# Optimization experiments

Hardware: AMD Instinct MI355X
Metric: run time of the kernel (lower is better)

The kernel has to match this reference:

```python
import math
import jax, jax.numpy as jnp
import numpy as np

D, H, NB, L, K = 45, 256, 6, 2, 8          # features, hidden, maf blocks, made hidden layers, spline bins
M = 3 * K - 1                               # params per feature (tails='linear')
TAIL = -math.log(1e-6)                      # tail_bound = -log(alpha)
MIN_BW = MIN_BH = MIN_D = 1e-3


def _masks():
    # nflows MADE sequential degrees (random_mask=False)
    d_in = np.arange(1, D + 1)
    d_h = (np.arange(H) % (D - 1)) + 1
    m0 = (d_h[:, None] >= d_in[None, :]).astype(np.float32)   # [H, D]
    mh = (d_h[:, None] >= d_h[None, :]).astype(np.float32)    # [H, H]
    d_out = np.repeat(d_in, M)                                 # nflows tile(): each degree repeated M times
    mf = (d_out[:, None] > d_h[None, :]).astype(np.float32)   # [D*M, H], strict for output layer
    return jnp.asarray(m0), jnp.asarray(mh), jnp.asarray(mf)


def _rq_spline(x, params):
    # x: [B, D]; params: [B, D, M]. unconstrained_rational_quadratic_spline, tails='linear'.
    uw = params[..., :K] / math.sqrt(H)        # nflows divides by sqrt(hidden_features)
    uh = params[..., K:2 * K] / math.sqrt(H)
    const = math.log(math.exp(1.0 - MIN_D) - 1.0)
    ud = jnp.pad(params[..., 2 * K:], ((0, 0), (0, 0), (1, 1)), constant_values=const)  # [B,D,K+1]
    inside = (x >= -TAIL) & (x <= TAIL)
    xc = jnp.clip(x, -TAIL, TAIL)

    def bin_edges(u, mn):
        p = jax.nn.softmax(u, -1)
        p = mn + (1.0 - mn * K) * p
        c = jnp.pad(jnp.cumsum(p, -1), ((0, 0), (0, 0), (1, 0)))
        c = 2.0 * TAIL * c - TAIL
        c = c.at[..., 0].set(-TAIL).at[..., -1].set(TAIL)
        return c, c[..., 1:] - c[..., :-1]

    cw, w = bin_edges(uw, MIN_BW)              # cumwidths [B,D,K+1], widths [B,D,K]
    ch, h = bin_edges(uh, MIN_BH)
    d = MIN_D + jax.nn.softplus(ud)            # derivatives [B,D,K+1]

    idx = jnp.clip(jnp.sum((xc[..., None] >= cw), -1) - 1, 0, K - 1)[..., None]
    g = lambda a: jnp.take_along_axis(a, idx, -1)[..., 0]
    icw, ibw, ich, ih = g(cw[..., :-1]), g(w), g(ch[..., :-1]), g(h)
    idelta = g(h / w)
    id0, id1 = g(d[..., :-1]), g(d[..., 1:])

    th = (xc - icw) / ibw
    th1 = th * (1.0 - th)
    den = idelta + (id0 + id1 - 2.0 * idelta) * th1
    y = ich + ih * (idelta * th * th + id0 * th1) / den
    lad = jnp.log(idelta * idelta * (id1 * th * th + 2.0 * idelta * th1 + id0 * (1.0 - th) ** 2)) - 2.0 * jnp.log(den)
    return jnp.where(inside, y, x), jnp.where(inside, lad, 0.0)


def setup_inputs() -> dict:
    key = jax.random.key(0)
    ks = jax.random.split(key, 10)
    B, s = 32768, 0.02
    return {
        "x": jax.random.normal(ks[0], (B, D), jnp.float32),
        "cond": jax.random.normal(ks[1], (B, 1), jnp.float32),
        "W0": jax.random.normal(ks[2], (NB, H, D), jnp.float32) * s,
        "b0": jax.random.normal(ks[3], (NB, H), jnp.float32) * s,
        "Wc": jax.random.normal(ks[4], (NB, H, 1), jnp.float32) * s,
        "bc": jax.random.normal(ks[5], (NB, H), jnp.float32) * s,
        "Wh": jax.random.normal(ks[6], (NB, L, H, H), jnp.float32) * s,
        "bh": jax.random.normal(ks[7], (NB, L, H), jnp.float32) * s,
        "Wf": jax.random.normal(ks[8], (NB, D * M, H), jnp.float32) * s,
        "bf": jax.random.normal(ks[9], (NB, D * M), jnp.float32) * s,
    }


def reference(x, cond, W0, b0, Wc, bc, Wh, bh, Wf, bf):
    m0, mh, mf = _masks()
    z = x
    ld = jnp.zeros(x.shape[0], x.dtype)
    for b in range(NB):  # CompositeTransform of NB MAF blocks
        hid = z @ (W0[b] * m0).T + b0[b] + cond @ Wc[b].T + bc[b]
        for l in range(L):  # MaskedFeedforwardBlock: linear -> ReLU (dropout=0, no BN)
            hid = jax.nn.relu(hid @ (Wh[b, l] * mh).T + bh[b, l])
        params = (hid @ (Wf[b] * mf).T + bf[b]).reshape(z.shape[0], D, M)
        z, lad = _rq_spline(z, params)
        ld = ld + lad.sum(-1)
    log_z = 0.5 * D * math.log(2.0 * math.pi)
    return -0.5 * jnp.sum(z * z, axis=1) - log_z + ld
```

## Files before the change

kernel.cpp:

```cpp
#include <hip/hip_runtime.h>


typedef __bf16 bf16;
typedef __bf16 bf16x8 __attribute__((ext_vector_type(8)));
typedef float  f32x16 __attribute__((ext_vector_type(16)));

#define TAILF  13.815510557964274f
#define LOGZ   41.352233994210265f

#define WS_W0M   0
#define WS_WHM   196608
#define WS_WFM   1769472
#define WS_BEFF  5210112
#define WS_BFP   5216256
#define WS_WCC   5243136
#define WS_NEED  5249280

#define N_W0  (6*256*64)
#define N_WH  (6*2*256*256)
#define N_WF  (6*5*224*256)
#define N_PREP (N_W0 + N_WH + N_WF)

__global__ void prep_all(const float* __restrict__ W0, const float* __restrict__ b0,
                         const float* __restrict__ Wc, const float* __restrict__ bc,
                         const float* __restrict__ Wh, const float* __restrict__ Wf,
                         const float* __restrict__ bfv,
                         bf16* __restrict__ W0m, bf16* __restrict__ Whm,
                         bf16* __restrict__ Wfm,
                         float* __restrict__ beff, float* __restrict__ bfp,
                         float* __restrict__ Wcc)
{
    int idx = blockIdx.x * 256 + threadIdx.x;
    if (idx < N_W0) {
        int j = idx & 7, lane = (idx >> 3) & 63, chunk = idx >> 9;
        int kt = chunk & 3, cg = (chunk >> 2) & 7, b = chunk >> 5;
        int col = cg * 32 + (lane & 31);
        int k   = kt * 16 + (lane >> 5) * 8 + j;
        float v = 0.f;
        if (k < 45 && (col % 44) >= k)
            v = W0[(b * 256 + col) * 45 + k];
        W0m[idx] = (bf16)v;
        if (k == 0) {
            beff[b * 256 + col] = b0[b * 256 + col] + bc[b * 256 + col];
            Wcc[b * 256 + col]  = Wc[b * 256 + col];
        }
    } else if (idx < N_W0 + N_WH) {
        int id = idx - N_W0;
        int j = id & 7, lane = (id >> 3) & 63, chunk = id >> 9;
        int kt = chunk & 15, cg = (chunk >> 4) & 7, bl = chunk >> 7;
        int col = cg * 32 + (lane & 31);
        int k   = kt * 16 + (lane >> 5) * 8 + j;
        float v = ((col % 44) >= (k % 44)) ? Wh[bl * 65536 + col * 256 + k] : 0.f;
        Whm[id] = (bf16)v;
    } else if (idx < N_PREP) {
        int id = idx - (N_W0 + N_WH);
        int j = id & 7, lane = (id >> 3) & 63, chunk = id >> 9;
        int kt = chunk & 15, t2 = chunk >> 4;
        int cg = t2 % 7, bg = t2 / 7;
        int b  = bg / 5, g = bg - 5 * b;
        int col = cg * 32 + (lane & 31);
        int k   = kt * 16 + (lane >> 5) * 8 + j;
        int f   = 9 * g + col / 23;
        int m   = col - (col / 23) * 23;
        bool valid = (col < 207);
        float v = 0.f;
        if (valid && (f > (k % 44)))
            v = Wf[(b * 1035 + f * 23 + m) * 256 + k];
        Wfm[id] = (bf16)v;
        if (k == 0)
            bfp[bg * 224 + col] = valid ? bfv[b * 1035 + f * 23 + m] : 0.f;
    }
}

#define SO_ZF    0
#define SO_ZB    11776
#define SO_HIDA  20992
#define SO_PBUF  54784
#define SO_COND  81408
#define SO_LD    81664
#define SMEM_BYTES 81920

template<int KT, int NACT, int MODE, int LIMIT>
__device__ __forceinline__ void gemm32(
    const bf16* Asrc, int lda,
    const bf16* __restrict__ Wp,
    const float* __restrict__ bias, const float* __restrict__ wcol,
    const float* condl, bf16* dst, int ldd,
    int w, int lane, bool preEpiSync)
{
    const bool act  = (w < NACT);
    const int  l31  = lane & 31;
    const int  kh8  = (lane >> 5) * 8;
    const bf16* Bp  = Wp + ((size_t)w * KT) * 512 + lane * 8;
    const bf16* Ap  = Asrc + l31 * lda + kh8;

    f32x16 acc0 = {}, acc1 = {};
    constexpr int CH = (KT < 8) ? KT : 8;
    #pragma unroll
    for (int khb = 0; khb < KT / CH; ++khb) {
        bf16x8 bq[CH];
        if (act) {
            #pragma unroll
            for (int c = 0; c < CH; ++c)
                bq[c] = *reinterpret_cast<const bf16x8*>(Bp + (khb * CH + c) * 512);
            #pragma unroll
            for (int c = 0; c < CH; ++c) {
                int kt = khb * CH + c;
                bf16x8 a0 = *reinterpret_cast<const bf16x8*>(Ap + kt * 16);
                bf16x8 a1 = *reinterpret_cast<const bf16x8*>(Ap + 32 * lda + kt * 16);
                acc0 = __builtin_amdgcn_mfma_f32_32x32x16_bf16(a0, bq[c], acc0, 0, 0, 0);
                acc1 = __builtin_amdgcn_mfma_f32_32x32x16_bf16(a1, bq[c], acc1, 0, 0, 0);
            }
        }
    }

    if (preEpiSync) __syncthreads();

    if (act) {
        const int col = w * 32 + l31;
        if (NACT == 8 || col < LIMIT) {
            const float bv  = bias[col];
            const float wcv = (MODE == 0) ? wcol[col] : 0.f;
            #pragma unroll
            for (int r = 0; r < 16; ++r) {
                int row = (r & 3) + 8 * (r >> 2) + (kh8 >> 1);
                float v0 = acc0[r] + bv;
                float v1 = acc1[r] + bv;
                if (MODE == 0) { v0 += condl[row] * wcv; v1 += condl[row + 32] * wcv; }
                if (MODE == 1) { v0 = fmaxf(v0, 0.f);   v1 = fmaxf(v1, 0.f); }
                dst[row * ldd + col]        = (bf16)v0;
                dst[(row + 32) * ldd + col] = (bf16)v1;
            }
        }
    }
    __syncthreads();
}

template<int NF>
__device__ __forceinline__ void do_spline(int fb, float* zf, bf16* zb,
                                          const bf16* pbuf, float* ldl, int t)
{
    for (int task = t; task < 64 * NF; task += 512) {
        int r  = task / NF;
        int fl = task - r * NF;
        const bf16* pp = pbuf + r * 208 + fl * 23;
        float P[23];
        #pragma unroll
        for (int m = 0; m < 23; ++m) P[m] = (float)pp[m];

        float xin = zf[r * 46 + fb + fl];
        float xc  = fminf(fmaxf(xin, -TAILF), TAILF);
        bool inside = (xin >= -TAILF) && (xin <= TAILF);

        float mw = P[0];
        #pragma unroll
        for (int i = 1; i < 8; ++i) mw = fmaxf(mw, P[i]);
        float ew[8], sw = 0.f;
        #pragma unroll
        for (int i = 0; i < 8; ++i) { ew[i] = __expf((P[i] - mw) * 0.0625f); sw += ew[i]; }
        float rws = 0.992f / sw;
        float cw[9]; cw[0] = -TAILF;
        #pragma unroll
        for (int i = 0; i < 8; ++i)
            cw[i + 1] = cw[i] + 2.f * TAILF * (1e-3f + ew[i] * rws);
        cw[8] = TAILF;
        float wb[8];
        #pragma unroll
        for (int i = 0; i < 8; ++i) wb[i] = cw[i + 1] - cw[i];

        float mh = P[8];
        #pragma unroll
        for (int i = 1; i < 8; ++i) mh = fmaxf(mh, P[8 + i]);
        float eh[8], sh = 0.f;
        #pragma unroll
        for (int i = 0; i < 8; ++i) { eh[i] = __expf((P[8 + i] - mh) * 0.0625f); sh += eh[i]; }
        float rhs = 0.992f / sh;
        float ch[9]; ch[0] = -TAILF;
        #pragma unroll
        for (int i = 0; i < 8; ++i)
            ch[i + 1] = ch[i] + 2.f * TAILF * (1e-3f + eh[i] * rhs);
        ch[8] = TAILF;
        float hb[8];
        #pragma unroll
        for (int i = 0; i < 8; ++i) hb[i] = ch[i + 1] - ch[i];

        float dd[9];
        dd[0] = 1.0f; dd[8] = 1.0f;
        #pragma unroll
        for (int i = 1; i < 8; ++i)
            dd[i] = 1e-3f + __logf(1.f + __expf(P[15 + i]));

        float icw = cw[0], ich = ch[0], ibw = wb[0], ibh = hb[0];
        float id0 = dd[0], id1 = dd[1];
        #pragma unroll
        for (int i = 1; i < 8; ++i) {
            bool ge = xc >= cw[i];
            icw = ge ? cw[i] : icw;  ich = ge ? ch[i] : ich;
            ibw = ge ? wb[i] : ibw;  ibh = ge ? hb[i] : ibh;
            id0 = ge ? dd[i] : id0;  id1 = ge ? dd[i + 1] : id1;
        }

        float th  = (xc - icw) / ibw;
        float th1 = th * (1.f - th);
        float dl  = ibh / ibw;
        float den = dl + (id0 + id1 - 2.f * dl) * th1;
        float yy  = ich + ibh * (dl * th * th + id0 * th1) / den;
        float num = dl * dl * (id1 * th * th + 2.f * dl * th1
                               + id0 * (1.f - th) * (1.f - th));
        float lad = __logf(num) - 2.f * __logf(den);

        if (inside) {
            zf[r * 46 + fb + fl] = yy;
            zb[r * 72 + fb + fl] = (bf16)yy;
            atomicAdd(&ldl[r], lad);
        }
    }
}

__global__ __launch_bounds__(512, 4) void maf_main(
    const float* __restrict__ x, const float* __restrict__ cond,
    const float* __restrict__ bh_all,
    const bf16* __restrict__ W0m, const bf16* __restrict__ Whm,
    const bf16* __restrict__ Wfm,
    const float* __restrict__ beff, const float* __restrict__ bfp,
    const float* __restrict__ Wcc,
    float* __restrict__ out, int B)
{
    extern __shared__ char smem[];
    float* zf    = (float*)(smem + SO_ZF);
    bf16*  zb    = (bf16*)(smem + SO_ZB);
    bf16*  hidA  = (bf16*)(smem + SO_HIDA);
    bf16*  pbuf  = (bf16*)(smem + SO_PBUF);
    float* condl = (float*)(smem + SO_COND);
    float* ldl   = (float*)(smem + SO_LD);

    const int t    = threadIdx.x;
    const int r0   = blockIdx.x * 64;
    const int w    = t >> 6;
    const int lane = t & 63;

    for (int i = t; i < 64 * 27; i += 512) {
        int r = i / 27, c = i - (i / 27) * 27;
        zb[r * 72 + 45 + c] = (bf16)0.f;
    }
    for (int i = t; i < 64 * 45; i += 512) {
        int r = i / 45, f = i - (i / 45) * 45;
        float v = (r0 + r < B) ? x[(size_t)(r0 + r) * 45 + f] : 0.f;
        zf[r * 46 + f] = v;
        zb[r * 72 + f] = (bf16)v;
    }
    if (t < 64) {
        condl[t] = (r0 + t < B) ? cond[r0 + t] : 0.f;
        ldl[t]   = 0.f;
    }
    __syncthreads();

    #pragma unroll 1
    for (int b = 0; b < 6; ++b) {
        gemm32<4, 8, 0, 256>(zb, 72, W0m + b * 16384,
                             beff + b * 256, Wcc + b * 256, condl,
                             hidA, 264, w, lane, false);
        #pragma unroll 1
        for (int l = 0; l < 2; ++l)
            gemm32<16, 8, 1, 256>(hidA, 264, Whm + (b * 2 + l) * 65536,
                                  bh_all + (b * 2 + l) * 256, nullptr, condl,
                                  hidA, 264, w, lane, true);
        #pragma unroll 1
        for (int g = 0; g < 5; ++g) {
            gemm32<16, 7, 2, 208>(hidA, 264, Wfm + (size_t)(b * 5 + g) * 57344,
                                  bfp + (b * 5 + g) * 224, nullptr, condl,
                                  pbuf, 208, w, lane, false);
            do_spline<9>(g * 9, zf, zb, pbuf, ldl, t);
            __syncthreads();
        }
    }

    if (t < 64 && r0 + t < B) {
        float s = 0.f;
        #pragma unroll
        for (int f = 0; f < 45; ++f) { float v = zf[t * 46 + f]; s += v * v; }
        out[r0 + t] = -0.5f * s - LOGZ + ldl[t];
    }
}

extern "C" void kernel_launch(void* const* d_in, const int* in_sizes, int n_in,
                              void* d_out, int out_size, void* d_ws, size_t ws_size,
                              hipStream_t stream)
{
    const float* x    = (const float*)d_in[0];
    const float* cond = (const float*)d_in[1];
    const float* W0   = (const float*)d_in[2];
    const float* b0   = (const float*)d_in[3];
    const float* Wc   = (const float*)d_in[4];
    const float* bc   = (const float*)d_in[5];
    const float* Wh   = (const float*)d_in[6];
    const float* bh   = (const float*)d_in[7];
    const float* Wf   = (const float*)d_in[8];
    const float* bfv  = (const float*)d_in[9];
    float* out = (float*)d_out;

    const int B = in_sizes[0] / 45;
    if (ws_size < (size_t)WS_NEED) return;

    char* ws = (char*)d_ws;
    bf16*  W0m  = (bf16*)(ws + WS_W0M);
    bf16*  Whm  = (bf16*)(ws + WS_WHM);
    bf16*  Wfm  = (bf16*)(ws + WS_WFM);
    float* beff = (float*)(ws + WS_BEFF);
    float* bfp  = (float*)(ws + WS_BFP);
    float* Wcc  = (float*)(ws + WS_WCC);

    prep_all<<<(N_PREP + 255) / 256, 256, 0, stream>>>(
        W0, b0, Wc, bc, Wh, Wf, bfv, W0m, Whm, Wfm, beff, bfp, Wcc);

    (void)hipFuncSetAttribute((const void*)maf_main,
                              hipFuncAttributeMaxDynamicSharedMemorySize,
                              SMEM_BYTES);

    const int nwg = (B + 63) / 64;
    maf_main<<<nwg, 512, SMEM_BYTES, stream>>>(
        x, cond, bh, W0m, Whm, Wfm, beff, bfp, Wcc, out, B);
}
```

Before: 372.9 us.

## Permute MADE hidden units by degree and skip masked-zero K tiles with balanced wave schedule

Hidden units are reordered so their MADE degrees are sorted, which turns the masked weight matrices into block-triangular form. Each GEMM now skips the k-tiles that are entirely zero, and per-wave schedule tables in constant memory spread the remaining tiles evenly across the 8 waves. The spline parameter buffer is also re-laid out so each thread reads 16-byte vectors, and per-row log-det sums go to a register instead of a shared atomic on every feature. The cost is more complex prep indexing, hand-tuned schedule tables that must match the masks exactly, and a runtime trip count in the inner loop.

```diff
diff --git a/kernel.cpp b/kernel.cpp
--- a/kernel.cpp
+++ b/kernel.cpp
@@ -14,21 +14,32 @@
 #define WS_BEFF  5210112
 #define WS_BFP   5216256
 #define WS_WCC   5243136
-#define WS_NEED  5249280
+#define WS_BHP   5249280
+#define WS_NEED  5261568
 
 #define N_W0  (6*256*64)
 #define N_WH  (6*2*256*256)
 #define N_WF  (6*5*224*256)
 #define N_PREP (N_W0 + N_WH + N_WF)
 
+__device__ __forceinline__ int s_deg(int s) {
+    return (s < 216) ? (s / 6) : (36 + (s - 216) / 5);
+}
+__device__ __forceinline__ int s_orig(int s) {
+    int d, rk;
+    if (s < 216) { d = s / 6; rk = s - d * 6; }
+    else { int u = s - 216; d = 36 + u / 5; rk = u - (u / 5) * 5; }
+    return d + 44 * rk;
+}
+
 __global__ void prep_all(const float* __restrict__ W0, const float* __restrict__ b0,
                          const float* __restrict__ Wc, const float* __restrict__ bc,
                          const float* __restrict__ Wh, const float* __restrict__ Wf,
-                         const float* __restrict__ bfv,
+                         const float* __restrict__ bfv, const float* __restrict__ bh,
                          bf16* __restrict__ W0m, bf16* __restrict__ Whm,
                          bf16* __restrict__ Wfm,
                          float* __restrict__ beff, float* __restrict__ bfp,
-                         float* __restrict__ Wcc)
+                         float* __restrict__ Wcc, float* __restrict__ bhp)
 {
     int idx = blockIdx.x * 256 + threadIdx.x;
     if (idx < N_W0) {
@@ -36,13 +47,14 @@
         int kt = chunk & 3, cg = (chunk >> 2) & 7, b = chunk >> 5;
         int col = cg * 32 + (lane & 31);
         int k   = kt * 16 + (lane >> 5) * 8 + j;
+        int o   = s_orig(col);
         float v = 0.f;
-        if (k < 45 && (col % 44) >= k)
-            v = W0[(b * 256 + col) * 45 + k];
+        if (k < 45 && s_deg(col) >= k)
+            v = W0[(b * 256 + o) * 45 + k];
         W0m[idx] = (bf16)v;
         if (k == 0) {
-            beff[b * 256 + col] = b0[b * 256 + col] + bc[b * 256 + col];
-            Wcc[b * 256 + col]  = Wc[b * 256 + col];
+            beff[b * 256 + col] = b0[b * 256 + o] + bc[b * 256 + o];
+            Wcc[b * 256 + col]  = Wc[b * 256 + o];
         }
     } else if (idx < N_W0 + N_WH) {
         int id = idx - N_W0;
@@ -50,8 +62,11 @@
         int kt = chunk & 15, cg = (chunk >> 4) & 7, bl = chunk >> 7;
         int col = cg * 32 + (lane & 31);
         int k   = kt * 16 + (lane >> 5) * 8 + j;
-        float v = ((col % 44) >= (k % 44)) ? Wh[bl * 65536 + col * 256 + k] : 0.f;
+        int oc  = s_orig(col), ok = s_orig(k);
+        float v = (s_deg(col) >= s_deg(k)) ? Wh[bl * 65536 + oc * 256 + ok] : 0.f;
         Whm[id] = (bf16)v;
+        if (k == 0)
+            bhp[bl * 256 + col] = bh[bl * 256 + oc];
     } else if (idx < N_PREP) {
         int id = idx - (N_W0 + N_WH);
         int j = id & 7, lane = (id >> 3) & 63, chunk = id >> 9;
@@ -60,12 +75,13 @@
         int b  = bg / 5, g = bg - 5 * b;
         int col = cg * 32 + (lane & 31);
         int k   = kt * 16 + (lane >> 5) * 8 + j;
+        int ok  = s_orig(k);
         int f   = 9 * g + col / 23;
         int m   = col - (col / 23) * 23;
         bool valid = (col < 207);
         float v = 0.f;
-        if (valid && (f > (k % 44)))
-            v = Wf[(b * 1035 + f * 23 + m) * 256 + k];
+        if (valid && (f > s_deg(k)))
+            v = Wf[(b * 1035 + f * 23 + m) * 256 + ok];
         Wfm[id] = (bf16)v;
         if (k == 0)
             bfp[bg * 224 + col] = valid ? bfv[b * 1035 + f * 23 + m] : 0.f;
@@ -74,79 +90,141 @@
 
 #define SO_ZF    0
 #define SO_ZB    11776
-#define SO_HIDA  20992
-#define SO_PBUF  54784
-#define SO_COND  81408
-#define SO_LD    81664
-#define SMEM_BYTES 81920
-
-template<int KT, int NACT, int MODE, int LIMIT>
+#define SO_HIDA  18944
+#define SO_PBUF  52736
+#define SO_COND  80528
+#define SO_LD    80784
+#define SMEM_BYTES 81040
+
+#define PBF 1544
+
+#define E2(c0,h0,k0,c1,h1,k1) \
+    ( (unsigned)(((k0)<<8)|((h0)<<5)|(c0)) | ((unsigned)(((k1)<<8)|((h1)<<5)|(c1))<<16) )
+
+__constant__ unsigned SCHED_IN[8] = {
+    E2(6,0,3, 0,0,1), E2(6,1,3, 0,1,1), E2(7,0,3, 1,0,1), E2(7,1,3, 1,1,1),
+    E2(3,0,2, 2,0,1), E2(3,1,2, 2,1,1), E2(4,0,2, 5,0,2), E2(4,1,2, 5,1,2)
+};
+__constant__ unsigned SCHED_HID[8] = {
+    E2(7,0,16, 0,0,3), E2(7,1,16, 0,1,3), E2(6,0,15, 1,0,5), E2(6,1,15, 1,1,5),
+    E2(5,0,12, 2,0,6), E2(5,1,12, 2,1,6), E2(4,0,11, 3,0,9), E2(4,1,11, 3,1,9)
+};
+__constant__ unsigned SCHED_OUT[5][8] = {
+  { E2(4,0,3, 0,0,1),  E2(4,1,3, 0,1,1),  E2(5,0,3, 1,0,1),  E2(5,1,3, 1,1,1),
+    E2(6,0,3, 31,0,0), E2(6,1,3, 31,0,0), E2(2,0,2, 2,1,2),  E2(3,0,2, 3,1,2) },
+  { E2(5,0,7, 0,0,4),  E2(5,1,7, 0,1,4),  E2(6,0,7, 31,0,0), E2(6,1,7, 31,0,0),
+    E2(3,0,6, 1,0,5),  E2(3,1,6, 1,1,5),  E2(4,0,6, 2,0,5),  E2(4,1,6, 2,1,5) },
+  { E2(5,0,10, 0,0,8), E2(5,1,10, 0,1,8), E2(6,0,10, 1,0,8), E2(6,1,10, 1,1,8),
+    E2(2,0,9, 2,1,9),  E2(3,0,9, 3,1,9),  E2(4,0,9, 31,0,0), E2(4,1,9, 31,0,0) },
+  { E2(5,0,14, 0,0,11),E2(5,1,14, 0,1,11),E2(6,0,14, 31,0,0),E2(6,1,14, 31,0,0),
+    E2(4,0,13, 1,0,11),E2(4,1,13, 1,1,11),E2(2,0,12, 2,1,12),E2(3,0,12, 3,1,12) },
+  { E2(3,0,16, 0,0,14),E2(3,1,16, 0,1,14),E2(4,0,16, 1,0,15),E2(4,1,16, 1,1,15),
+    E2(5,0,16, 2,0,15),E2(5,1,16, 2,1,15),E2(6,0,16, 31,0,0),E2(6,1,16, 31,0,0) }
+};
+
+template<int MODE>
+__device__ __forceinline__ void epi32(const f32x16& acc, int cg, int hf,
+    const float* __restrict__ bias, const float* __restrict__ wcol,
+    const float* condl, bf16* dst, int l31, int kh8)
+{
+    const int col = cg * 32 + l31;
+    if (MODE == 2 && col >= 207) return;
+    const float bv = bias[col];
+    const int rb = (kh8 >> 1) + hf * 32;
+    if (MODE == 2) {
+        const int fl = col / 23, m = col - fl * 23;
+        bf16* dp = dst + fl * PBF + m;
+        #pragma unroll
+        for (int r = 0; r < 16; ++r) {
+            int row = (r & 3) + 8 * (r >> 2) + rb;
+            dp[row * 24] = (bf16)(acc[r] + bv);
+        }
+    } else {
+        const float wcv = (MODE == 0) ? wcol[col] : 0.f;
+        #pragma unroll
+        for (int r = 0; r < 16; ++r) {
+            int row = (r & 3) + 8 * (r >> 2) + rb;
+            float v = acc[r] + bv;
+            if (MODE == 0) v += condl[row] * wcv;
+            if (MODE == 1) v = fmaxf(v, 0.f);
+            dst[row * 264 + col] = (bf16)v;
+        }
+    }
+}
+
+template<int KTFULL, int MODE>
 __device__ __forceinline__ void gemm32(
-    const bf16* Asrc, int lda,
+    const bf16* Asrc, const int lda,
     const bf16* __restrict__ Wp,
     const float* __restrict__ bias, const float* __restrict__ wcol,
-    const float* condl, bf16* dst, int ldd,
+    const float* condl, bf16* dst,
+    const unsigned* __restrict__ sched,
     int w, int lane, bool preEpiSync)
 {
-    const bool act  = (w < NACT);
-    const int  l31  = lane & 31;
-    const int  kh8  = (lane >> 5) * 8;
-    const bf16* Bp  = Wp + ((size_t)w * KT) * 512 + lane * 8;
-    const bf16* Ap  = Asrc + l31 * lda + kh8;
+    const int l31 = lane & 31;
+    const int kh8 = (lane >> 5) * 8;
+    const unsigned se = sched[__builtin_amdgcn_readfirstlane(w)];
+    const int cg0 = se & 31,         hf0 = (se >> 5) & 1,  kt0 = (se >> 8) & 31;
+    const int cg1 = (se >> 16) & 31, hf1 = (se >> 21) & 1, kt1 = (se >> 24) & 31;
 
     f32x16 acc0 = {}, acc1 = {};
-    constexpr int CH = (KT < 8) ? KT : 8;
-    #pragma unroll
-    for (int khb = 0; khb < KT / CH; ++khb) {
-        bf16x8 bq[CH];
-        if (act) {
+    {
+        const bf16* Bp = Wp + (size_t)cg0 * (KTFULL * 512) + lane * 8;
+        const bf16* Ap = Asrc + (hf0 * 32 + l31) * lda + kh8;
+        #pragma unroll 1
+        for (int kb = 0; kb < kt0; kb += 4) {
+            bf16x8 bq[4], aq[4];
             #pragma unroll
-            for (int c = 0; c < CH; ++c)
-                bq[c] = *reinterpret_cast<const bf16x8*>(Bp + (khb * CH + c) * 512);
+            for (int c = 0; c < 4; ++c) if (kb + c < kt0) {
+                bq[c] = *reinterpret_cast<const bf16x8*>(Bp + (kb + c) * 512);
+                aq[c] = *reinterpret_cast<const bf16x8*>(Ap + (kb + c) * 16);
+            }
             #pragma unroll
-            for (int c = 0; c < CH; ++c) {
-                int kt = khb * CH + c;
-                bf16x8 a0 = *reinterpret_cast<const bf16x8*>(Ap + kt * 16);
-                bf16x8 a1 = *reinterpret_cast<const bf16x8*>(Ap + 32 * lda + kt * 16);
-                acc0 = __builtin_amdgcn_mfma_f32_32x32x16_bf16(a0, bq[c], acc0, 0, 0, 0);
-                acc1 = __builtin_amdgcn_mfma_f32_32x32x16_bf16(a1, bq[c], acc1, 0, 0, 0);
+            for (int c = 0; c < 4; ++c) if (kb + c < kt0)
+                acc0 = __builtin_amdgcn_mfma_f32_32x32x16_bf16(aq[c], bq[c], acc0, 0, 0, 0);
+        }
+    }
+    {
+        const bf16* Bp = Wp + (size_t)cg1 * (KTFULL * 512) + lane * 8;
+        const bf16* Ap = Asrc + (hf1 * 32 + l31) * lda + kh8;
+        #pragma unroll 1
+        for (int kb = 0; kb < kt1; kb += 4) {
+            bf16x8 bq[4], aq[4];
+            #pragma unroll
+            for (int c = 0; c < 4; ++c) if (kb + c < kt1) {
+                bq[c] = *reinterpret_cast<const bf16x8*>(Bp + (kb + c) * 512);
+                aq[c] = *reinterpret_cast<const bf16x8*>(Ap + (kb + c) * 16);
             }
+            #pragma unroll
+            for (int c = 0; c < 4; ++c) if (kb + c < kt1)
+                acc1 = __builtin_amdgcn_mfma_f32_32x32x16_bf16(aq[c], bq[c], acc1, 0, 0, 0);
         }
     }
 
     if (preEpiSync) __syncthreads();
 
-    if (act) {
-        const int col = w * 32 + l31;
-        if (NACT == 8 || col < LIMIT) {
-            const float bv  = bias[col];
-            const float wcv = (MODE == 0) ? wcol[col] : 0.f;
-            #pragma unroll
-            for (int r = 0; r < 16; ++r) {
-                int row = (r & 3) + 8 * (r >> 2) + (kh8 >> 1);
-                float v0 = acc0[r] + bv;
-                float v1 = acc1[r] + bv;
-                if (MODE == 0) { v0 += condl[row] * wcv; v1 += condl[row + 32] * wcv; }
-                if (MODE == 1) { v0 = fmaxf(v0, 0.f);   v1 = fmaxf(v1, 0.f); }
-                dst[row * ldd + col]        = (bf16)v0;
-                dst[(row + 32) * ldd + col] = (bf16)v1;
-            }
-        }
-    }
+    if (cg0 != 31) epi32<MODE>(acc0, cg0, hf0, bias, wcol, condl, dst, l31, kh8);
+    if (cg1 != 31) epi32<MODE>(acc1, cg1, hf1, bias, wcol, condl, dst, l31, kh8);
     __syncthreads();
 }
 
-template<int NF>
-__device__ __forceinline__ void do_spline(int fb, float* zf, bf16* zb,
-                                          const bf16* pbuf, float* ldl, int t)
-{
-    for (int task = t; task < 64 * NF; task += 512) {
-        int r  = task / NF;
-        int fl = task - r * NF;
-        const bf16* pp = pbuf + r * 208 + fl * 23;
+__device__ __forceinline__ void do_spline9(int fb, float* zf, bf16* zb,
+                                           const bf16* pbuf, int t, float& lad_acc)
+{
+    #pragma unroll 1
+    for (int task = t; task < 576; task += 512) {
+        int fl = task >> 6, r = task & 63;
+        const bf16* pp = pbuf + fl * PBF + r * 24;
+        bf16x8 q0 = *reinterpret_cast<const bf16x8*>(pp);
+        bf16x8 q1 = *reinterpret_cast<const bf16x8*>(pp + 8);
+        bf16x8 q2 = *reinterpret_cast<const bf16x8*>(pp + 16);
         float P[23];
         #pragma unroll
-        for (int m = 0; m < 23; ++m) P[m] = (float)pp[m];
+        for (int m = 0; m < 8; ++m) P[m]      = (float)q0[m];
+        #pragma unroll
+        for (int m = 0; m < 8; ++m) P[8 + m]  = (float)q1[m];
+        #pragma unroll
+        for (int m = 0; m < 7; ++m) P[16 + m] = (float)q2[m];
 
         float xin = zf[r * 46 + fb + fl];
         float xc  = fminf(fmaxf(xin, -TAILF), TAILF);
@@ -211,19 +289,18 @@
 
         if (inside) {
             zf[r * 46 + fb + fl] = yy;
-            zb[r * 72 + fb + fl] = (bf16)yy;
-            atomicAdd(&ldl[r], lad);
-        }
+            zb[r * 56 + fb + fl] = (bf16)yy;
+        }
+        lad_acc += inside ? lad : 0.f;
     }
 }
 
 __global__ __launch_bounds__(512, 4) void maf_main(
     const float* __restrict__ x, const float* __restrict__ cond,
-    const float* __restrict__ bh_all,
     const bf16* __restrict__ W0m, const bf16* __restrict__ Whm,
     const bf16* __restrict__ Wfm,
     const float* __restrict__ beff, const float* __restrict__ bfp,
-    const float* __restrict__ Wcc,
+    const float* __restrict__ Wcc, const float* __restrict__ bhp,
     float* __restrict__ out, int B)
 {
     extern __shared__ char smem[];
@@ -239,15 +316,15 @@
     const int w    = t >> 6;
     const int lane = t & 63;
 
-    for (int i = t; i < 64 * 27; i += 512) {
-        int r = i / 27, c = i - (i / 27) * 27;
-        zb[r * 72 + 45 + c] = (bf16)0.f;
+    for (int i = t; i < 64 * 11; i += 512) {
+        int r = i / 11, c = i - (i / 11) * 11;
+        zb[r * 56 + 45 + c] = (bf16)0.f;
     }
     for (int i = t; i < 64 * 45; i += 512) {
         int r = i / 45, f = i - (i / 45) * 45;
         float v = (r0 + r < B) ? x[(size_t)(r0 + r) * 45 + f] : 0.f;
         zf[r * 46 + f] = v;
-        zb[r * 72 + f] = (bf16)v;
+        zb[r * 56 + f] = (bf16)v;
     }
     if (t < 64) {
         condl[t] = (r0 + t < B) ? cond[r0 + t] : 0.f;
@@ -255,25 +332,30 @@
     }
     __syncthreads();
 
+    float lad_acc = 0.f;
+
     #pragma unroll 1
     for (int b = 0; b < 6; ++b) {
-        gemm32<4, 8, 0, 256>(zb, 72, W0m + b * 16384,
-                             beff + b * 256, Wcc + b * 256, condl,
-                             hidA, 264, w, lane, false);
+        gemm32<4, 0>(zb, 56, W0m + b * 16384,
+                     beff + b * 256, Wcc + b * 256, condl,
+                     hidA, SCHED_IN, w, lane, false);
         #pragma unroll 1
         for (int l = 0; l < 2; ++l)
-            gemm32<16, 8, 1, 256>(hidA, 264, Whm + (b * 2 + l) * 65536,
-                                  bh_all + (b * 2 + l) * 256, nullptr, condl,
-                                  hidA, 264, w, lane, true);
+            gemm32<16, 1>(hidA, 264, Whm + (b * 2 + l) * 65536,
+                          bhp + (b * 2 + l) * 256, nullptr, condl,
+                          hidA, SCHED_HID, w, lane, true);
         #pragma unroll 1
         for (int g = 0; g < 5; ++g) {
-            gemm32<16, 7, 2, 208>(hidA, 264, Wfm + (size_t)(b * 5 + g) * 57344,
-                                  bfp + (b * 5 + g) * 224, nullptr, condl,
-                                  pbuf, 208, w, lane, false);
-            do_spline<9>(g * 9, zf, zb, pbuf, ldl, t);
+            gemm32<16, 2>(hidA, 264, Wfm + (size_t)(b * 5 + g) * 57344,
+                          bfp + (b * 5 + g) * 224, nullptr, condl,
+                          pbuf, SCHED_OUT[g], w, lane, false);
+            do_spline9(g * 9, zf, zb, pbuf, t, lad_acc);
             __syncthreads();
         }
     }
+
+    atomicAdd(&ldl[t & 63], lad_acc);
+    __syncthreads();
 
     if (t < 64 && r0 + t < B) {
         float s = 0.f;
@@ -309,9 +391,10 @@
     float* beff = (float*)(ws + WS_BEFF);
     float* bfp  = (float*)(ws + WS_BFP);
     float* Wcc  = (float*)(ws + WS_WCC);
+    float* bhp  = (float*)(ws + WS_BHP);
 
     prep_all<<<(N_PREP + 255) / 256, 256, 0, stream>>>(
-        W0, b0, Wc, bc, Wh, Wf, bfv, W0m, Whm, Wfm, beff, bfp, Wcc);
+        W0, b0, Wc, bc, Wh, Wf, bfv, bh, W0m, Whm, Wfm, beff, bfp, Wcc, bhp);
 
     (void)hipFuncSetAttribute((const void*)maf_main,
                               hipFuncAttributeMaxDynamicSharedMemorySize,
@@ -319,5 +402,5 @@
 
     const int nwg = (B + 63) / 64;
     maf_main<<<nwg, 512, SMEM_BYTES, stream>>>(
-        x, cond, bh, W0m, Whm, Wfm, beff, bfp, Wcc, out, B);
-}
+        x, cond, W0m, Whm, Wfm, beff, bfp, Wcc, bhp, out, B);
+}
```

After: 366.9 us. Within noise of the previous version (-1.6%).
